# Kernel optimization log

Measured on AMD Instinct MI355X. Metric: run time of the kernel, lower is better.

Reference implementation:

```python
import jax, jax.numpy as jnp
import numpy as np


def setup_inputs() -> dict:
    key = jax.random.key(0)
    ks = jax.random.split(key, 6)
    b, h, w, m, d = 8, 32, 32, 8, 64
    c = m * d
    return {
        "x": jax.random.normal(ks[0], (b, h, w, c), jnp.float32),
        "qkv_w": jax.random.normal(ks[1], (d, 3 * d), jnp.float32) * np.float32(1.0 / np.sqrt(d)),
        "qkv_b": jnp.zeros((3 * d,), jnp.float32),
        # HeNormal over (2h-1)^2 scalar table
        "pos_emb": jax.random.normal(ks[2], ((2 * h - 1) ** 2,), jnp.float32) * np.float32(np.sqrt(2.0 / (2 * h - 1) ** 2)),
        "ht_w": jax.random.normal(ks[3], (c, c), jnp.float32) * np.float32(1.0 / np.sqrt(c)),
        "ht_b": jnp.zeros((c,), jnp.float32),
    }


def _rel_pos_idx(h):
    # Static Swin-style 2D relative position index, shape (h*h, h*h)
    coords = jnp.arange(h)
    base = coords[None, :] - coords[:, None]          # base[a, b] = b - a
    horiz = jnp.tile(base, (h, h))                    # (h^2, h^2)
    vert = jnp.repeat(jnp.repeat(base, h, axis=0), h, axis=1)
    return (2 * h - 1) * (vert + h - 1) + (horiz + h - 1)


def reference(x, qkv_w, qkv_b, pos_emb, ht_w, ht_b):
    b, h, w, c = x.shape
    d = qkv_w.shape[0]
    m = c // d
    hw = h * w
    # split channels into heads: (b, m, hw, d)
    xh = x.reshape(b, h, w, m, d).transpose(0, 3, 1, 2, 4).reshape(b, m, hw, d)
    # 1x1 conv == per-position linear, then channel layout (d, 3) as in the TF reshape
    qkv = (xh @ qkv_w + qkv_b).reshape(b, m, hw, d, 3)
    q, k, v = qkv[..., 0], qkv[..., 1], qkv[..., 2]
    q = q / jnp.sqrt(jnp.float32(d))
    att = jnp.einsum('bmic,bmjc->bmij', q, k)         # (b, m, hw, hw)
    att = att + pos_emb[_rel_pos_idx(h)]              # bias shared across batch & heads
    att = jax.nn.softmax(att, axis=-1)
    out = jnp.einsum('bmij,bmjc->bmic', att, v)       # (b, m, hw, d)
    out = out.reshape(b, m, h, w, d).transpose(0, 2, 3, 1, 4).reshape(b, h, w, c)
    return out @ ht_w + ht_b
```

## Files before the change

### kernel.cpp

```cpp
#include <hip/hip_runtime.h>

#define Dd 64
#define Cc 512
#define HW 1024
#define BM 64
#define LOG2E 1.44269504f

typedef __attribute__((ext_vector_type(8))) short bf16x8;
typedef __attribute__((ext_vector_type(4))) short bf16x4;
typedef __attribute__((ext_vector_type(4))) float f32x4;

__device__ __forceinline__ unsigned short f2bf(float f) {
  unsigned int u = __builtin_bit_cast(unsigned int, f);
  u += 0x7fffu + ((u >> 16) & 1u);
  return (unsigned short)(u >> 16);
}

__device__ __forceinline__ unsigned int pack2(float lo, float hi) {
  return (unsigned int)f2bf(lo) | ((unsigned int)f2bf(hi) << 16);
}

__device__ __forceinline__ int swz(int row, int cb) {
  return row * 128 + (cb ^ ((row & 7) << 4));
}

__global__ __launch_bounds__(256, 2) void qkv_kernel(
    const float* __restrict__ x, const float* __restrict__ w,
    const float* __restrict__ bqkv,
    unsigned short* __restrict__ Q, unsigned short* __restrict__ K,
    unsigned short* __restrict__ Vt) {
  __shared__ unsigned short Wt[192 * 64];
  __shared__ float bl[192];
  char* WtB = (char*)Wt;
  int t = threadIdx.x, lane = t & 63, wv = t >> 6;
  int c = lane & 15, r4 = lane >> 4;
  int bm = blockIdx.x >> 4;
  int pos0 = (blockIdx.x & 15) * 64;
  int bb = bm >> 3, mm = bm & 7;

  for (int idx = t; idx < 12288; idx += 256) {
    int k = idx / 192, col = idx - (idx / 192) * 192;
    int d3 = col / 3, which = col - d3 * 3;
    int np = which * 64 + d3;
    float v = w[idx];
    if (which == 0) v *= 0.125f;
    *(unsigned short*)(WtB + np * 128 + ((k * 2) ^ ((np & 7) << 4))) = f2bf(v);
  }
  if (t < 192) {
    int d3 = t / 3, which = t - d3 * 3;
    float bvv = bqkv[t];
    if (which == 0) bvv *= 0.125f;
    bl[which * 64 + d3] = bvv;
  }
  __syncthreads();

  bf16x8 af[12][2];
#pragma unroll
  for (int nf = 0; nf < 12; ++nf) {
    int row = nf * 16 + c, sw = (row & 7) << 4;
#pragma unroll
    for (int kc = 0; kc < 2; ++kc)
      af[nf][kc] = *(const bf16x8*)(WtB + row * 128 + ((kc * 64 + r4 * 16) ^ sw));
  }
  f32x4 acc[12];
#pragma unroll
  for (int nf = 0; nf < 12; ++nf)
    acc[nf] = *(const f32x4*)&bl[nf * 16 + r4 * 4];

  int pos = pos0 + wv * 16 + c;
  const float* xr = x + (size_t)(bb * HW + pos) * Cc + mm * Dd;
  bf16x8 xb[2];
#pragma unroll
  for (int kc = 0; kc < 2; ++kc) {
    f32x4 lo = *(const f32x4*)(xr + kc * 32 + r4 * 8);
    f32x4 hi = *(const f32x4*)(xr + kc * 32 + r4 * 8 + 4);
    union { unsigned int u[4]; bf16x8 b; } cv;
    cv.u[0] = pack2(lo[0], lo[1]);
    cv.u[1] = pack2(lo[2], lo[3]);
    cv.u[2] = pack2(hi[0], hi[1]);
    cv.u[3] = pack2(hi[2], hi[3]);
    xb[kc] = cv.b;
  }
#pragma unroll
  for (int nf = 0; nf < 12; ++nf) {
    acc[nf] = __builtin_amdgcn_mfma_f32_16x16x32_bf16(af[nf][0], xb[0], acc[nf], 0, 0, 0);
    acc[nf] = __builtin_amdgcn_mfma_f32_16x16x32_bf16(af[nf][1], xb[1], acc[nf], 0, 0, 0);
  }
  size_t obase = ((size_t)bm * HW + pos) * Dd;
#pragma unroll
  for (int nf = 0; nf < 8; ++nf) {
    unsigned int d0 = pack2(acc[nf][0], acc[nf][1]);
    unsigned int d1 = pack2(acc[nf][2], acc[nf][3]);
    unsigned long long wd = (unsigned long long)d0 | ((unsigned long long)d1 << 32);
    unsigned short* dst = (nf < 4) ? Q : K;
    *(unsigned long long*)(dst + obase + (nf & 3) * 16 + r4 * 4) = wd;
  }
#pragma unroll
  for (int nf = 8; nf < 12; ++nf) {
#pragma unroll
    for (int reg = 0; reg < 4; ++reg) {
      int d = (nf - 8) * 16 + r4 * 4 + reg;
      Vt[((size_t)bm * Dd + d) * HW + pos] = f2bf(acc[nf][reg]);
    }
  }
}

__global__ __launch_bounds__(256, 2) void attn_kernel(
    const unsigned short* __restrict__ Q, const unsigned short* __restrict__ K,
    const unsigned short* __restrict__ Vt, const float* __restrict__ pe,
    unsigned short* __restrict__ O) {
  __shared__ unsigned short Kt[64 * 64];
  __shared__ unsigned short Vl[64 * 64];
  __shared__ unsigned short Pl[4][2048];
  __shared__ float pes[3969];
  char* KtB = (char*)Kt;
  char* VtB = (char*)Vl;
  char* PlB = (char*)Pl;
  int t = threadIdx.x, lane = t & 63, wv = t >> 6;
  int c = lane & 15, r4 = lane >> 4;
  int swzid = (blockIdx.x & 7) * 64 + (blockIdx.x >> 3);
  int bm = swzid >> 3;
  int i0 = (swzid & 7) * 128;
  for (int i = t; i < 3969; i += 256) pes[i] = pe[i];

  const unsigned short* Qb = Q + ((size_t)bm * HW + i0 + wv * 32) * Dd;
  bf16x8 qb[2][2];
#pragma unroll
  for (int h = 0; h < 2; ++h)
#pragma unroll
    for (int kc = 0; kc < 2; ++kc)
      qb[h][kc] = *(const bf16x8*)(Qb + (h * 16 + c) * Dd + kc * 32 + r4 * 8);

  int hb[2];
#pragma unroll
  for (int h = 0; h < 2; ++h) {
    int ibase = i0 + wv * 32 + h * 16;
    int yi = ibase >> 5, xib = ibase & 31;
    hb[h] = 63 * (31 - yi) + 31 - xib - c + r4 * 4;
  }

  f32x4 oacc[2][4];
  float m_run[2], l_run[2];
#pragma unroll
  for (int h = 0; h < 2; ++h) {
    m_run[h] = -1e30f;
    l_run[h] = 0.f;
#pragma unroll
    for (int nf = 0; nf < 4; ++nf) oacc[h][nf] = {0.f, 0.f, 0.f, 0.f};
  }

  const unsigned short* Kg = K + (size_t)bm * HW * Dd;
  const unsigned short* Vg = Vt + (size_t)bm * Dd * HW;
  char* pb = PlB + wv * 4096;
  int swp = (c & 7) << 4;
  int srow = t >> 3, sc8 = t & 7;

  bf16x8 kreg[2], vreg[2];
  auto issue = [&](int j0) {
#pragma unroll
    for (int rep = 0; rep < 2; ++rep) {
      int row = srow + rep * 32;
      kreg[rep] = *(const bf16x8*)(Kg + (size_t)(j0 + row) * Dd + sc8 * 8);
      vreg[rep] = *(const bf16x8*)(Vg + (size_t)row * HW + j0 + sc8 * 8);
    }
  };

  issue(0);
  for (int jt = 0; jt < 16; ++jt) {
    int j0 = jt * 64;
    __syncthreads();
#pragma unroll
    for (int rep = 0; rep < 2; ++rep) {
      int row = srow + rep * 32;
      *(bf16x8*)(KtB + swz(row, sc8 * 16)) = kreg[rep];
      *(bf16x8*)(VtB + swz(row, sc8 * 16)) = vreg[rep];
    }
    __syncthreads();
    if (jt < 15) issue(j0 + 64);

    f32x4 sacc[2][4];
#pragma unroll
    for (int h = 0; h < 2; ++h) {
      int tb = hb[h] + 63 * (j0 >> 5);
#pragma unroll
      for (int jf = 0; jf < 4; ++jf) {
        int o = tb + (jf >> 1) * 63 + (jf & 1) * 16;
        sacc[h][jf] = {pes[o], pes[o + 1], pes[o + 2], pes[o + 3]};
      }
    }
#pragma unroll
    for (int jf = 0; jf < 4; ++jf) {
      int row = jf * 16 + c, sw = (row & 7) << 4;
      bf16x8 kb0 = *(const bf16x8*)(KtB + row * 128 + ((r4 * 16) ^ sw));
      bf16x8 kb1 = *(const bf16x8*)(KtB + row * 128 + ((64 + r4 * 16) ^ sw));
#pragma unroll
      for (int h = 0; h < 2; ++h) {
        sacc[h][jf] = __builtin_amdgcn_mfma_f32_16x16x32_bf16(kb0, qb[h][0], sacc[h][jf], 0, 0, 0);
        sacc[h][jf] = __builtin_amdgcn_mfma_f32_16x16x32_bf16(kb1, qb[h][1], sacc[h][jf], 0, 0, 0);
      }
    }
#pragma unroll
    for (int h = 0; h < 2; ++h) {
      float mx = fmaxf(
          fmaxf(fmaxf(fmaxf(sacc[h][0][0], sacc[h][0][1]), fmaxf(sacc[h][0][2], sacc[h][0][3])),
                fmaxf(fmaxf(sacc[h][1][0], sacc[h][1][1]), fmaxf(sacc[h][1][2], sacc[h][1][3]))),
          fmaxf(fmaxf(fmaxf(sacc[h][2][0], sacc[h][2][1]), fmaxf(sacc[h][2][2], sacc[h][2][3])),
                fmaxf(fmaxf(sacc[h][3][0], sacc[h][3][1]), fmaxf(sacc[h][3][2], sacc[h][3][3]))));
      mx = fmaxf(mx, __shfl_xor(mx, 16));
      mx = fmaxf(mx, __shfl_xor(mx, 32));
      float mnew = fmaxf(m_run[h], mx);
      float sc = __builtin_amdgcn_exp2f((m_run[h] - mnew) * LOG2E);
      m_run[h] = mnew;
      l_run[h] *= sc;
#pragma unroll
      for (int nf = 0; nf < 4; ++nf) oacc[h][nf] *= sc;
      float ml = mnew * LOG2E;
      float ps = 0.f;
#pragma unroll
      for (int jf = 0; jf < 4; ++jf)
#pragma unroll
        for (int r = 0; r < 4; ++r) {
          float p = __builtin_amdgcn_exp2f(fmaf(sacc[h][jf][r], LOG2E, -ml));
          sacc[h][jf][r] = p;
          ps += p;
        }
      ps += __shfl_xor(ps, 16);
      ps += __shfl_xor(ps, 32);
      l_run[h] += ps;
      char* pbh = pb + h * 2048 + c * 128;
#pragma unroll
      for (int jf = 0; jf < 4; ++jf) {
        unsigned int w0 = pack2(sacc[h][jf][0], sacc[h][jf][1]);
        unsigned int w1 = pack2(sacc[h][jf][2], sacc[h][jf][3]);
        unsigned long long wd = (unsigned long long)w0 | ((unsigned long long)w1 << 32);
        *(unsigned long long*)(pbh + ((jf * 32 + r4 * 8) ^ swp)) = wd;
      }
    }
#pragma unroll
    for (int jk = 0; jk < 2; ++jk) {
      bf16x8 pa[2];
#pragma unroll
      for (int h = 0; h < 2; ++h)
        pa[h] = *(const bf16x8*)(pb + h * 2048 + c * 128 +
                                 ((jk * 64 + r4 * 16) ^ swp));
#pragma unroll
      for (int nf = 0; nf < 4; ++nf) {
        int row = nf * 16 + c, sw = (row & 7) << 4;
        bf16x8 vb = *(const bf16x8*)(VtB + row * 128 + ((jk * 64 + r4 * 16) ^ sw));
        oacc[0][nf] = __builtin_amdgcn_mfma_f32_16x16x32_bf16(vb, pa[0], oacc[0][nf], 0, 0, 0);
        oacc[1][nf] = __builtin_amdgcn_mfma_f32_16x16x32_bf16(vb, pa[1], oacc[1][nf], 0, 0, 0);
      }
    }
  }

  __syncthreads();
  char* zone = ((wv < 2) ? KtB : VtB) + (wv & 1) * 4096;
  float inv0 = 1.f / l_run[0], inv1 = 1.f / l_run[1];
#pragma unroll
  for (int h = 0; h < 2; ++h) {
    float inv = h ? inv1 : inv0;
    int row = h * 16 + c, sw = (row & 7) << 4;
#pragma unroll
    for (int nf = 0; nf < 4; ++nf) {
      unsigned int d0 = pack2(oacc[h][nf][0] * inv, oacc[h][nf][1] * inv);
      unsigned int d1 = pack2(oacc[h][nf][2] * inv, oacc[h][nf][3] * inv);
      unsigned long long wd = (unsigned long long)d0 | ((unsigned long long)d1 << 32);
      *(unsigned long long*)(zone + row * 128 + ((nf * 32 + r4 * 8) ^ sw)) = wd;
    }
  }
  __syncthreads();
  int rrow = lane >> 1, half = lane & 1;
  int sw = (rrow & 7) << 4;
  size_t obase = ((size_t)bm * HW + i0 + wv * 32 + rrow) * Dd + half * 32;
#pragma unroll
  for (int q = 0; q < 4; ++q) {
    bf16x8 vv = *(const bf16x8*)(zone + rrow * 128 + ((half * 64 + q * 16) ^ sw));
    *(bf16x8*)(O + obase + q * 8) = vv;
  }
}

__global__ __launch_bounds__(256) void proj_kernel(
    const unsigned short* __restrict__ O, const float* __restrict__ W,
    const float* __restrict__ bias, float* __restrict__ out) {
  __shared__ unsigned short Aq[128 * 64];
  __shared__ unsigned short Bt[64 * 64];
  char* AqB = (char*)Aq;
  char* BtB = (char*)Bt;
  int t = threadIdx.x, lane = t & 63, wv = t >> 6;
  int rb = blockIdx.x >> 3, n0 = (blockIdx.x & 7) * 64;
  int row0 = rb * 128;
  int b = row0 >> 10, pos0 = row0 & 1023;
  int c = lane & 15, r4 = lane >> 4;
  int nt = t & 15, kt = t >> 4;

  f32x4 acc[2][4];
#pragma unroll
  for (int g = 0; g < 2; ++g)
#pragma unroll
    for (int nf = 0; nf < 4; ++nf) acc[g][nf] = {0.f, 0.f, 0.f, 0.f};

  bf16x8 areg[4];
  f32x4 wreg[4];

  auto issue = [&](int m) {
#pragma unroll
    for (int rep = 0; rep < 4; ++rep) {
      int cid = t + rep * 256;
      int row = cid >> 3, c8 = cid & 7;
      areg[rep] = *(const bf16x8*)(O + ((size_t)(b * 8 + m) * HW + pos0 + row) * Dd + c8 * 8);
    }
#pragma unroll
    for (int r = 0; r < 4; ++r)
      wreg[r] = *(const f32x4*)(W + (size_t)(m * 64 + kt * 4 + r) * Cc + n0 + nt * 4);
  };

  issue(0);
  for (int m = 0; m < 8; ++m) {
    __syncthreads();
#pragma unroll
    for (int rep = 0; rep < 4; ++rep) {
      int cid = t + rep * 256;
      int row = cid >> 3, c8 = cid & 7;
      *(bf16x8*)(AqB + swz(row, c8 * 16)) = areg[rep];
    }
#pragma unroll
    for (int e = 0; e < 4; ++e) {
      bf16x4 bt = {(short)f2bf(wreg[0][e]), (short)f2bf(wreg[1][e]),
                   (short)f2bf(wreg[2][e]), (short)f2bf(wreg[3][e])};
      *(bf16x4*)(BtB + swz(nt * 4 + e, kt * 8)) = bt;
    }
    __syncthreads();
    if (m < 7) issue(m + 1);

#pragma unroll
    for (int kc = 0; kc < 2; ++kc) {
      bf16x8 a0 = *(const bf16x8*)(AqB + swz(wv * 32 + c, kc * 64 + r4 * 16));
      bf16x8 a1 = *(const bf16x8*)(AqB + swz(wv * 32 + 16 + c, kc * 64 + r4 * 16));
#pragma unroll
      for (int nf = 0; nf < 4; ++nf) {
        bf16x8 bb = *(const bf16x8*)(BtB + swz(nf * 16 + c, kc * 64 + r4 * 16));
        acc[0][nf] = __builtin_amdgcn_mfma_f32_16x16x32_bf16(a0, bb, acc[0][nf], 0, 0, 0);
        acc[1][nf] = __builtin_amdgcn_mfma_f32_16x16x32_bf16(a1, bb, acc[1][nf], 0, 0, 0);
      }
    }
  }

  float bv[4];
#pragma unroll
  for (int nf = 0; nf < 4; ++nf) bv[nf] = bias[n0 + nf * 16 + c];
#pragma unroll
  for (int g = 0; g < 2; ++g) {
#pragma unroll
    for (int reg = 0; reg < 4; ++reg) {
      int row = row0 + wv * 32 + g * 16 + r4 * 4 + reg;
#pragma unroll
      for (int nf = 0; nf < 4; ++nf)
        out[(size_t)row * Cc + n0 + nf * 16 + c] = acc[g][nf][reg] + bv[nf];
    }
  }
}

extern "C" void kernel_launch(void* const* d_in, const int* in_sizes, int n_in,
                              void* d_out, int out_size, void* d_ws, size_t ws_size,
                              hipStream_t stream) {
  const float* x      = (const float*)d_in[0];
  const float* qkv_w  = (const float*)d_in[1];
  const float* qkv_b  = (const float*)d_in[2];
  const float* pos_emb= (const float*)d_in[3];
  const float* ht_w   = (const float*)d_in[4];
  const float* ht_b   = (const float*)d_in[5];
  float* out = (float*)d_out;

  const size_t NQ = (size_t)BM * HW * Dd;
  unsigned short* Qw  = (unsigned short*)d_ws;
  unsigned short* Kw  = Qw + NQ;
  unsigned short* Vtw = Kw + NQ;
  unsigned short* Ow  = Vtw + NQ;

  hipLaunchKernelGGL(qkv_kernel, dim3(1024), dim3(256), 0, stream,
                     x, qkv_w, qkv_b, Qw, Kw, Vtw);
  hipLaunchKernelGGL(attn_kernel, dim3(512), dim3(256), 0, stream,
                     Qw, Kw, Vtw, pos_emb, Ow);
  hipLaunchKernelGGL(proj_kernel, dim3(512), dim3(256), 0, stream,
                     Ow, ht_w, ht_b, out);
}
```

Measured before the change: 78.17 us.

## Double-buffer K/V tiles, read bias from global, and skip softmax rescale lazily

Doubles the K and V shared-memory tiles so the next tile is staged after compute, which leaves one barrier per iteration instead of two. Drops the 16KB shared copy of the position-bias table and reads the bias straight from global/L1, freeing LDS that the extra buffers take. Adds a lazy online-softmax rescale that only updates the running max when some lane's new max exceeds the old one by more than 8. That skips the exp and the accumulator scaling in most iterations, at the cost of larger unnormalized exponent values.

Measured after the change: 72.89 us. 1.07x faster.

```diff
diff --git a/kernel.cpp b/kernel.cpp
--- a/kernel.cpp
+++ b/kernel.cpp
@@ -109,19 +109,15 @@
     const unsigned short* __restrict__ Q, const unsigned short* __restrict__ K,
     const unsigned short* __restrict__ Vt, const float* __restrict__ pe,
     unsigned short* __restrict__ O) {
-  __shared__ unsigned short Kt[64 * 64];
-  __shared__ unsigned short Vl[64 * 64];
+  __shared__ unsigned short Kt[2][64 * 64];
+  __shared__ unsigned short Vl[2][64 * 64];
   __shared__ unsigned short Pl[4][2048];
-  __shared__ float pes[3969];
-  char* KtB = (char*)Kt;
-  char* VtB = (char*)Vl;
   char* PlB = (char*)Pl;
   int t = threadIdx.x, lane = t & 63, wv = t >> 6;
   int c = lane & 15, r4 = lane >> 4;
   int swzid = (blockIdx.x & 7) * 64 + (blockIdx.x >> 3);
   int bm = swzid >> 3;
   int i0 = (swzid & 7) * 128;
-  for (int i = t; i < 3969; i += 256) pes[i] = pe[i];
 
   const unsigned short* Qb = Q + ((size_t)bm * HW + i0 + wv * 32) * Dd;
   bf16x8 qb[2][2];
@@ -164,19 +160,25 @@
       vreg[rep] = *(const bf16x8*)(Vg + (size_t)row * HW + j0 + sc8 * 8);
     }
   };
+  auto stage = [&](int buf) {
+#pragma unroll
+    for (int rep = 0; rep < 2; ++rep) {
+      int row = srow + rep * 32;
+      *(bf16x8*)((char*)Kt[buf] + swz(row, sc8 * 16)) = kreg[rep];
+      *(bf16x8*)((char*)Vl[buf] + swz(row, sc8 * 16)) = vreg[rep];
+    }
+  };
 
   issue(0);
+  stage(0);
+  issue(64);
+  __syncthreads();
+
+  int cur = 0;
   for (int jt = 0; jt < 16; ++jt) {
     int j0 = jt * 64;
-    __syncthreads();
-#pragma unroll
-    for (int rep = 0; rep < 2; ++rep) {
-      int row = srow + rep * 32;
-      *(bf16x8*)(KtB + swz(row, sc8 * 16)) = kreg[rep];
-      *(bf16x8*)(VtB + swz(row, sc8 * 16)) = vreg[rep];
-    }
-    __syncthreads();
-    if (jt < 15) issue(j0 + 64);
+    char* KtB = (char*)Kt[cur];
+    char* VtB = (char*)Vl[cur];
 
     f32x4 sacc[2][4];
 #pragma unroll
@@ -185,7 +187,7 @@
 #pragma unroll
       for (int jf = 0; jf < 4; ++jf) {
         int o = tb + (jf >> 1) * 63 + (jf & 1) * 16;
-        sacc[h][jf] = {pes[o], pes[o + 1], pes[o + 2], pes[o + 3]};
+        sacc[h][jf] = {pe[o], pe[o + 1], pe[o + 2], pe[o + 3]};
       }
     }
 #pragma unroll
@@ -208,13 +210,15 @@
                 fmaxf(fmaxf(sacc[h][3][0], sacc[h][3][1]), fmaxf(sacc[h][3][2], sacc[h][3][3]))));
       mx = fmaxf(mx, __shfl_xor(mx, 16));
       mx = fmaxf(mx, __shfl_xor(mx, 32));
-      float mnew = fmaxf(m_run[h], mx);
-      float sc = __builtin_amdgcn_exp2f((m_run[h] - mnew) * LOG2E);
-      m_run[h] = mnew;
-      l_run[h] *= sc;
-#pragma unroll
-      for (int nf = 0; nf < 4; ++nf) oacc[h][nf] *= sc;
-      float ml = mnew * LOG2E;
+      if (!__all(mx <= m_run[h] + 8.f)) {
+        float mnew = fmaxf(m_run[h], mx);
+        float sc = __builtin_amdgcn_exp2f((m_run[h] - mnew) * LOG2E);
+        m_run[h] = mnew;
+        l_run[h] *= sc;
+#pragma unroll
+        for (int nf = 0; nf < 4; ++nf) oacc[h][nf] *= sc;
+      }
+      float ml = m_run[h] * LOG2E;
       float ps = 0.f;
 #pragma unroll
       for (int jf = 0; jf < 4; ++jf)
@@ -251,10 +255,16 @@
         oacc[1][nf] = __builtin_amdgcn_mfma_f32_16x16x32_bf16(vb, pa[1], oacc[1][nf], 0, 0, 0);
       }
     }
+    if (jt < 15) {
+      stage(cur ^ 1);
+      if (jt < 14) issue(j0 + 128);
+      __syncthreads();
+      cur ^= 1;
+    }
   }
 
   __syncthreads();
-  char* zone = ((wv < 2) ? KtB : VtB) + (wv & 1) * 4096;
+  char* zone = ((wv < 2) ? (char*)Kt[0] : (char*)Vl[0]) + (wv & 1) * 4096;
   float inv0 = 1.f / l_run[0], inv1 = 1.f / l_run[1];
 #pragma unroll
   for (int h = 0; h < 2; ++h) {
```
